# Kernel optimization log

Hardware: AMD Instinct MI355X
Metric: run time of the kernel (lower is better)

The kernel has to match this reference:

```python
import jax, jax.numpy as jnp
import numpy as np

V = 32000      # vocab_size
D = 768        # embed_dim / d_model
NL = 2         # attn_layers
BATCH = 2
T = 1024       # seq_len
ED = 2 * D     # d_inner (expand_factor=2)
NS = 16        # d_state
K = 4          # d_conv
DT_RANK = (D + 15) // 16  # ceil(d_model/16) = 48


def setup_inputs():
    key = jax.random.key(0)
    ks = jax.random.split(key, 12)
    nrm = lambda k, shp, s=0.02: (jax.random.normal(k, shp, jnp.float32) * s)
    tokens = jax.random.randint(ks[0], (BATCH, T), 0, V)
    embed = nrm(ks[1], (V, D))
    in_proj_w = nrm(ks[2], (NL, 2 * ED, D))
    conv_w = nrm(ks[3], (NL, ED, 1, K), 0.1)   # depthwise conv kernel (O=ED, I/g=1, K)
    conv_b = jnp.zeros((NL, ED), jnp.float32)
    x_proj_w = nrm(ks[4], (NL, DT_RANK + 2 * NS, ED))
    dt_proj_w = nrm(ks[5], (NL, ED, DT_RANK), 0.05)
    dt_proj_b = nrm(ks[6], (NL, ED), 0.05)
    # S4D real init: A = -[1..NS] per channel
    A_log = jnp.log(jnp.broadcast_to(jnp.arange(1, NS + 1, dtype=jnp.float32), (NL, ED, NS)))
    D_param = jnp.ones((NL, ED), jnp.float32)
    out_proj_w = nrm(ks[7], (NL, D, ED))
    ln_w = jnp.ones((NL, D), jnp.float32)
    ln_b = jnp.zeros((NL, D), jnp.float32)
    head_w = nrm(ks[8], (V, D))
    head_b = jnp.zeros((V,), jnp.float32)
    return {"tokens": tokens, "embed": embed, "in_proj_w": in_proj_w,
            "conv_w": conv_w, "conv_b": conv_b, "x_proj_w": x_proj_w,
            "dt_proj_w": dt_proj_w, "dt_proj_b": dt_proj_b, "A_log": A_log,
            "D_param": D_param, "out_proj_w": out_proj_w, "ln_w": ln_w,
            "ln_b": ln_b, "head_w": head_w, "head_b": head_b}


def silu(x):
    return x * jax.nn.sigmoid(x)


def layer_norm(x, w, b, eps=1e-5):
    mu = jnp.mean(x, axis=-1, keepdims=True)
    var = jnp.mean(jnp.square(x - mu), axis=-1, keepdims=True)
    return (x - mu) * jax.lax.rsqrt(var + eps) * w + b


def mamba_block(x, in_w, cw, cb, xp_w, dt_w, dt_b, a_log, d_par, out_w):
    # x: (B, T, D)
    xz = jnp.einsum('btd,ed->bte', x, in_w)           # (B, T, 2*ED)
    xin, z = jnp.split(xz, 2, axis=-1)                 # each (B, T, ED)
    # causal depthwise conv over time
    xc = jnp.transpose(xin, (0, 2, 1))                 # (B, ED, T)
    xc = jax.lax.conv_general_dilated(
        xc, cw, window_strides=(1,), padding=[(K - 1, 0)],
        dimension_numbers=('NCH', 'OIH', 'NCH'), feature_group_count=ED)
    xc = xc + cb[None, :, None]
    xin = silu(jnp.transpose(xc, (0, 2, 1)))           # (B, T, ED)
    # selective SSM
    A = -jnp.exp(a_log)                                # (ED, NS)
    dbc = jnp.einsum('bte,fe->btf', xin, xp_w)         # (B, T, dt_rank + 2*NS)
    delta = dbc[..., :DT_RANK]
    Bm = dbc[..., DT_RANK:DT_RANK + NS]                # (B, T, NS)
    Cm = dbc[..., DT_RANK + NS:]                       # (B, T, NS)
    delta = jax.nn.softplus(jnp.einsum('btr,er->bte', delta, dt_w) + dt_b)  # (B, T, ED)
    dA = jnp.exp(delta[..., None] * A)                 # (B, T, ED, NS)
    dBx = (delta * xin)[..., None] * Bm[:, :, None, :] # (B, T, ED, NS)

    def step(h, inp):
        dA_t, dBx_t, C_t = inp                         # (B,ED,NS),(B,ED,NS),(B,NS)
        h = dA_t * h + dBx_t
        y = jnp.einsum('ben,bn->be', h, C_t)
        return h, y

    h0 = jnp.zeros((x.shape[0], ED, NS), xin.dtype)
    _, ys = jax.lax.scan(step, h0,
                         (jnp.swapaxes(dA, 0, 1), jnp.swapaxes(dBx, 0, 1),
                          jnp.swapaxes(Cm, 0, 1)))
    y = jnp.swapaxes(ys, 0, 1) + d_par * xin           # (B, T, ED)
    return jnp.einsum('bte,de->btd', y * silu(z), out_w)


def reference(tokens, embed, in_proj_w, conv_w, conv_b, x_proj_w, dt_proj_w,
              dt_proj_b, A_log, D_param, out_proj_w, ln_w, ln_b, head_w, head_b):
    x = embed[tokens]                                  # (B, T, D)
    for l in range(NL):  # note: NO residual, matches x = ln(layer(x))
        x = layer_norm(
            mamba_block(x, in_proj_w[l], conv_w[l], conv_b[l], x_proj_w[l],
                        dt_proj_w[l], dt_proj_b[l], A_log[l], D_param[l],
                        out_proj_w[l]),
            ln_w[l], ln_b[l])
    return jnp.einsum('btd,vd->btv', x, head_w) + head_b
```

## Files before the change

### kernel.cpp

```cpp
#include <hip/hip_runtime.h>
#include <hip/hip_bf16.h>
#include <cstdint>
#include <cstddef>

using u16 = unsigned short;

#define DEV static __device__ __forceinline__

DEV float bf2f(u16 u) {
  unsigned int x = ((unsigned int)u) << 16;
  float f;
  __builtin_memcpy(&f, &x, 4);
  return f;
}

DEV u16 f2bf(float f) {
  unsigned int x;
  __builtin_memcpy(&x, &f, 4);
  unsigned int r = (x + 0x7fffu + ((x >> 16) & 1u)) >> 16;
  return (u16)r;
}

typedef __bf16 bf16x8 __attribute__((ext_vector_type(8)));
typedef float f32x4 __attribute__((ext_vector_type(4)));

DEV f32x4 mfma_bf16(bf16x8 a, bf16x8 b, f32x4 c) {
  return __builtin_amdgcn_mfma_f32_16x16x32_bf16(a, b, c, 0, 0, 0);
}

DEV void async_ld16(const void* g, void* lds) {
  __builtin_amdgcn_global_load_lds((const __attribute__((address_space(1))) void*)g,
                                   (__attribute__((address_space(3))) void*)lds,
                                   16, 0, 0);
}

__global__ __launch_bounds__(256) void k_cvt(const float* __restrict__ src,
                                             u16* __restrict__ dst, int n) {
  for (int i = blockIdx.x * 256 + threadIdx.x; i < n; i += gridDim.x * 256)
    dst[i] = f2bf(src[i]);
}

__global__ __launch_bounds__(256) void k_zero(float* __restrict__ p, int n) {
  const int i = blockIdx.x * 256 + threadIdx.x;
  if (i < n) p[i] = 0.f;
}

template <bool SPLIT, bool BIAS>
__global__ __launch_bounds__(512, 2) void gemm2(
    const u16* __restrict__ Ahi, const u16* __restrict__ Alo,
    const u16* __restrict__ Bw, float* __restrict__ Cf,
    const float* __restrict__ bias, int M, int N, int K, int ldc) {
  __shared__ __align__(16) u16 sA[2][128 * 64];
  __shared__ __align__(16) u16 sAl[SPLIT ? 2 : 1][128 * 64];
  __shared__ __align__(16) u16 sB[2][256 * 64];

  const int tid = threadIdx.x;
  const int wave = tid >> 6;
  const int lane = tid & 63;
  const int nwg = gridDim.x;
  const int w = (blockIdx.x & 7) * (nwg >> 3) + (blockIdx.x >> 3);
  const int mBlocks = M >> 7;
  const int mb = w % mBlocks;
  const int nb = w / mBlocks;
  const int mBase = mb * 128;
  const int nBase = nb * 256;
  const int wm = wave >> 2;
  const int wn = wave & 3;

  f32x4 acc[4][4];
#pragma unroll
  for (int i = 0; i < 4; ++i)
#pragma unroll
    for (int j = 0; j < 4; ++j) acc[i][j] = f32x4{0.f, 0.f, 0.f, 0.f};

  const int rl = lane >> 3;
  const int sw = (lane & 7) ^ rl;

  auto stage = [&](int bf, int k0) {
    const int koff = k0 + sw * 8;
#pragma unroll
    for (int r = 0; r < 2; ++r) {
      const int row = r * 64 + wave * 8;
      async_ld16(Ahi + (size_t)(mBase + row + rl) * K + koff,
                 (u16*)sA[bf] + row * 64);
    }
    if constexpr (SPLIT) {
#pragma unroll
      for (int r = 0; r < 2; ++r) {
        const int row = r * 64 + wave * 8;
        async_ld16(Alo + (size_t)(mBase + row + rl) * K + koff,
                   (u16*)sAl[bf] + row * 64);
      }
    }
#pragma unroll
    for (int r = 0; r < 4; ++r) {
      const int row = r * 64 + wave * 8;
      async_ld16(Bw + (size_t)(nBase + row + rl) * K + koff,
                 (u16*)sB[bf] + row * 64);
    }
  };

  const int rr = lane & 15;
  const int qh = lane >> 4;

  stage(0, 0);
  __syncthreads();

  const int nt = K >> 6;
  int cur = 0;
  for (int t = 0; t < nt; ++t) {
    if (t + 1 < nt) stage(cur ^ 1, (t + 1) * 64);
#pragma unroll
    for (int ph = 0; ph < 4; ++ph) {
      const int ks = (ph >> 1) * 32;
      const int ih = (ph & 1) * 2;
      const int q = (ks >> 3) + qh;
      bf16x8 aH[2], aL[2], bF[4];
#pragma unroll
      for (int i = 0; i < 2; ++i) {
        const int ra = wm * 64 + (ih + i) * 16 + rr;
        const int off = ra * 64 + ((q ^ (ra & 7)) << 3);
        aH[i] = *(const bf16x8*)((const u16*)sA[cur] + off);
        if constexpr (SPLIT) aL[i] = *(const bf16x8*)((const u16*)sAl[cur] + off);
      }
#pragma unroll
      for (int j = 0; j < 4; ++j) {
        const int rb = wn * 64 + j * 16 + rr;
        bF[j] = *(const bf16x8*)((const u16*)sB[cur] + rb * 64 + ((q ^ (rb & 7)) << 3));
      }
      __builtin_amdgcn_s_setprio(1);
#pragma unroll
      for (int i = 0; i < 2; ++i)
#pragma unroll
        for (int j = 0; j < 4; ++j) {
          acc[ih + i][j] = mfma_bf16(aH[i], bF[j], acc[ih + i][j]);
          if constexpr (SPLIT) acc[ih + i][j] = mfma_bf16(aL[i], bF[j], acc[ih + i][j]);
        }
      __builtin_amdgcn_s_setprio(0);
    }
    __syncthreads();
    cur ^= 1;
  }

  const int r0 = (lane >> 4) * 4;
  const int cn = lane & 15;
#pragma unroll
  for (int i = 0; i < 4; ++i) {
    const int mm = mBase + wm * 64 + i * 16 + r0;
#pragma unroll
    for (int j = 0; j < 4; ++j) {
      const int nn = nBase + wn * 64 + j * 16 + cn;
      float bv = 0.f;
      if constexpr (BIAS) bv = bias[nn];
#pragma unroll
      for (int r = 0; r < 4; ++r)
        Cf[(size_t)(mm + r) * ldc + nn] = acc[i][j][r] + bv;
    }
  }
}

template <bool SPLIT, bool BIAS, bool ATOMIC>
__global__ __launch_bounds__(256, 2) void gemm_bt(
    const u16* __restrict__ Ahi, const u16* __restrict__ Alo,
    const u16* __restrict__ Bw, float* __restrict__ Cf,
    const float* __restrict__ bias, int M, int N, int K, int ldc, int kChunk) {
  __shared__ __align__(16) u16 sA[128 * 64];
  __shared__ __align__(16) u16 sB[128 * 64];
  __shared__ __align__(16) u16 sAl[SPLIT ? 128 * 64 : 8];

  const int tid = threadIdx.x;
  const int wave = tid >> 6;
  const int lane = tid & 63;
  const int mBase = blockIdx.y * 128;
  const int nBase = blockIdx.x * 128;
  const int kBeg = blockIdx.z * kChunk;
  const int wm = wave >> 1;
  const int wn = wave & 1;

  f32x4 acc[4][4];
#pragma unroll
  for (int i = 0; i < 4; ++i)
#pragma unroll
    for (int j = 0; j < 4; ++j) acc[i][j] = f32x4{0.f, 0.f, 0.f, 0.f};

  const int rsub = lane >> 3;
  const int ksub = (lane & 7) * 8;

  for (int k0 = kBeg; k0 < kBeg + kChunk; k0 += 64) {
#pragma unroll
    for (int it = 0; it < 4; ++it) {
      const int chunk = it * 4 + wave;
      const int row = chunk * 8 + rsub;
      async_ld16(Ahi + (size_t)(mBase + row) * K + (k0 + ksub), (char*)sA + chunk * 1024);
      if constexpr (SPLIT)
        async_ld16(Alo + (size_t)(mBase + row) * K + (k0 + ksub), (char*)sAl + chunk * 1024);
      int rn = nBase + row;
      if (rn > N - 1) rn = N - 1;
      async_ld16(Bw + (size_t)rn * K + (k0 + ksub), (char*)sB + chunk * 1024);
    }
    __syncthreads();

    const int rr = lane & 15;
    const int q8 = (lane >> 4) * 8;
#pragma unroll
    for (int ks = 0; ks < 64; ks += 32) {
      bf16x8 aH[4], bF[4], aL[4];
#pragma unroll
      for (int i = 0; i < 4; ++i) {
        aH[i] = *(const bf16x8*)(sA + (wm * 64 + i * 16 + rr) * 64 + ks + q8);
        bF[i] = *(const bf16x8*)(sB + (wn * 64 + i * 16 + rr) * 64 + ks + q8);
        if constexpr (SPLIT)
          aL[i] = *(const bf16x8*)(sAl + (wm * 64 + i * 16 + rr) * 64 + ks + q8);
      }
#pragma unroll
      for (int i = 0; i < 4; ++i)
#pragma unroll
        for (int j = 0; j < 4; ++j) {
          acc[i][j] = mfma_bf16(aH[i], bF[j], acc[i][j]);
          if constexpr (SPLIT) acc[i][j] = mfma_bf16(aL[i], bF[j], acc[i][j]);
        }
    }
    __syncthreads();
  }

  const int r0 = (lane >> 4) * 4;
  const int cn = lane & 15;
#pragma unroll
  for (int i = 0; i < 4; ++i) {
    const int mm = mBase + wm * 64 + i * 16 + r0;
#pragma unroll
    for (int j = 0; j < 4; ++j) {
      const int nn = nBase + wn * 64 + j * 16 + cn;
      if (nn < N) {
        float bv = 0.f;
        if constexpr (BIAS) bv = bias[nn];
#pragma unroll
        for (int r = 0; r < 4; ++r) {
          if constexpr (ATOMIC)
            atomicAdd(&Cf[(size_t)(mm + r) * ldc + nn], acc[i][j][r]);
          else
            Cf[(size_t)(mm + r) * ldc + nn] = acc[i][j][r] + bv;
        }
      }
    }
  }
}

__global__ __launch_bounds__(256) void k_embed(const int* __restrict__ tok,
                                               const float* __restrict__ emb,
                                               u16* __restrict__ xh,
                                               u16* __restrict__ xl) {
  const int m = blockIdx.x;
  const float* src = emb + (size_t)tok[m] * 768;
  for (int d = threadIdx.x; d < 768; d += 256) {
    const float v = src[d];
    const u16 h = f2bf(v);
    xh[(size_t)m * 768 + d] = h;
    xl[(size_t)m * 768 + d] = f2bf(v - bf2f(h));
  }
}

__global__ __launch_bounds__(256) void k_conv(const float* __restrict__ xz,
                                              const float* __restrict__ cw,
                                              const float* __restrict__ cb,
                                              float* __restrict__ xinc,
                                              u16* __restrict__ xih,
                                              u16* __restrict__ xil) {
  const int idx = blockIdx.x * 256 + threadIdx.x;
  const int e = idx % 1536;
  const int m = idx / 1536;
  const int t = m & 1023;
  const int b = m >> 10;
  float acc = cb[e];
#pragma unroll
  for (int k = 0; k < 4; ++k) {
    const int tt = t - 3 + k;
    if (tt >= 0) acc += xz[(size_t)((b << 10) + tt) * 3072 + e] * cw[e * 4 + k];
  }
  const float s = acc / (1.f + __expf(-acc));
  xinc[idx] = s;
  const u16 h = f2bf(s);
  xih[idx] = h;
  xil[idx] = f2bf(s - bf2f(h));
}

__global__ __launch_bounds__(256) void k_dt(const float* __restrict__ dbc,
                                            const float* __restrict__ dtw,
                                            const float* __restrict__ dtb,
                                            float* __restrict__ delta) {
  const int m = blockIdx.x;
  __shared__ float sd[48];
  if (threadIdx.x < 48) sd[threadIdx.x] = dbc[m * 80 + threadIdx.x];
  __syncthreads();
  for (int e = threadIdx.x; e < 1536; e += 256) {
    float acc = dtb[e];
#pragma unroll
    for (int r = 0; r < 48; ++r) acc += sd[r] * dtw[e * 48 + r];
    const float sp = (acc > 20.f) ? acc : log1pf(__expf(acc));
    delta[m * 1536 + e] = sp;
  }
}

#define SCAN_NC 16
#define SCAN_CL 64

__global__ __launch_bounds__(256) void k_scan1(
    const float* __restrict__ delta, const float* __restrict__ xinc,
    const float* __restrict__ dbc, const float* __restrict__ alog,
    float* __restrict__ chP, float* __restrict__ chQ) {
  const int b = blockIdx.y;
  const int c = blockIdx.z;
  const int e = blockIdx.x * 16 + (threadIdx.x >> 4);
  const int n = threadIdx.x & 15;
  const float Aen = -__expf(alog[e * 16 + n]);
  const int m0 = (b << 10) + c * SCAN_CL;
  float h = 0.f, P = 1.f;
  float dl = delta[m0 * 1536 + e];
  float xi = xinc[m0 * 1536 + e];
  float Bn = dbc[m0 * 80 + 48 + n];
  for (int t = 0; t < SCAN_CL; ++t) {
    const float dl_c = dl, xi_c = xi, Bn_c = Bn;
    if (t < SCAN_CL - 1) {
      const int m2 = m0 + t + 1;
      dl = delta[m2 * 1536 + e];
      xi = xinc[m2 * 1536 + e];
      Bn = dbc[m2 * 80 + 48 + n];
    }
    const float dA = __expf(dl_c * Aen);
    P *= dA;
    h = dA * h + (dl_c * xi_c) * Bn_c;
  }
  const size_t idx = (((size_t)b * SCAN_NC + c) * 1536 + e) * 16 + n;
  chP[idx] = P;
  chQ[idx] = h;
}

__global__ __launch_bounds__(256) void k_scan_fix(const float* __restrict__ chP,
                                                  const float* __restrict__ chQ,
                                                  float* __restrict__ hst) {
  const int b = blockIdx.y;
  const int e = blockIdx.x * 16 + (threadIdx.x >> 4);
  const int n = threadIdx.x & 15;
  float h = 0.f;
#pragma unroll
  for (int c = 0; c < SCAN_NC; ++c) {
    const size_t idx = (((size_t)b * SCAN_NC + c) * 1536 + e) * 16 + n;
    hst[idx] = h;
    h = chP[idx] * h + chQ[idx];
  }
}

__global__ __launch_bounds__(256) void k_scan2(
    const float* __restrict__ delta, const float* __restrict__ xinc,
    const float* __restrict__ dbc, const float* __restrict__ xz,
    const float* __restrict__ alog, const float* __restrict__ dpar,
    const float* __restrict__ hst, u16* __restrict__ ymh,
    u16* __restrict__ yml) {
  const int b = blockIdx.y;
  const int c = blockIdx.z;
  const int e = blockIdx.x * 16 + (threadIdx.x >> 4);
  const int n = threadIdx.x & 15;
  const float Aen = -__expf(alog[e * 16 + n]);
  const float dp = dpar[e];
  const int m0 = (b << 10) + c * SCAN_CL;
  float h = hst[(((size_t)b * SCAN_NC + c) * 1536 + e) * 16 + n];
  float dl = delta[m0 * 1536 + e];
  float xi = xinc[m0 * 1536 + e];
  float Bn = dbc[m0 * 80 + 48 + n];
  float Cn = dbc[m0 * 80 + 64 + n];
  float zz = xz[(size_t)m0 * 3072 + 1536 + e];
  for (int t = 0; t < SCAN_CL; ++t) {
    const float dl_c = dl, xi_c = xi, Bn_c = Bn, Cn_c = Cn, zz_c = zz;
    if (t < SCAN_CL - 1) {
      const int m2 = m0 + t + 1;
      dl = delta[m2 * 1536 + e];
      xi = xinc[m2 * 1536 + e];
      Bn = dbc[m2 * 80 + 48 + n];
      Cn = dbc[m2 * 80 + 64 + n];
      zz = xz[(size_t)m2 * 3072 + 1536 + e];
    }
    const float dA = __expf(dl_c * Aen);
    h = dA * h + (dl_c * xi_c) * Bn_c;
    float p = h * Cn_c;
    p += __shfl_xor(p, 1);
    p += __shfl_xor(p, 2);
    p += __shfl_xor(p, 4);
    p += __shfl_xor(p, 8);
    if (n == 0) {
      const float y = p + dp * xi_c;
      const float sz = zz_c / (1.f + __expf(-zz_c));
      const float ym = y * sz;
      const int mt = m0 + t;
      const u16 hh = f2bf(ym);
      ymh[mt * 1536 + e] = hh;
      yml[mt * 1536 + e] = f2bf(ym - bf2f(hh));
    }
  }
}

__global__ __launch_bounds__(256) void k_ln(const float* __restrict__ g,
                                            const float* __restrict__ w,
                                            const float* __restrict__ bb,
                                            u16* __restrict__ xh,
                                            u16* __restrict__ xl) {
  const int m = blockIdx.x;
  const float* row = g + (size_t)m * 768;
  const int tid = threadIdx.x;
  const float v0 = row[tid], v1 = row[tid + 256], v2 = row[tid + 512];
  float s = v0 + v1 + v2;
#pragma unroll
  for (int o = 32; o > 0; o >>= 1) s += __shfl_xor(s, o);
  __shared__ float red[4];
  if ((tid & 63) == 0) red[tid >> 6] = s;
  __syncthreads();
  const float mu = (red[0] + red[1] + red[2] + red[3]) * (1.f / 768.f);
  const float d0 = v0 - mu, d1 = v1 - mu, d2 = v2 - mu;
  float q = d0 * d0 + d1 * d1 + d2 * d2;
#pragma unroll
  for (int o = 32; o > 0; o >>= 1) q += __shfl_xor(q, o);
  __syncthreads();
  if ((tid & 63) == 0) red[tid >> 6] = q;
  __syncthreads();
  const float var = (red[0] + red[1] + red[2] + red[3]) * (1.f / 768.f);
  const float rs = rsqrtf(var + 1e-5f);
  const float dd[3] = {d0, d1, d2};
#pragma unroll
  for (int i = 0; i < 3; ++i) {
    const int d = tid + i * 256;
    const float y = dd[i] * rs * w[d] + bb[d];
    const u16 h = f2bf(y);
    xh[(size_t)m * 768 + d] = h;
    xl[(size_t)m * 768 + d] = f2bf(y - bf2f(h));
  }
}

extern "C" void kernel_launch(void* const* d_in, const int* in_sizes, int n_in,
                              void* d_out, int out_size, void* d_ws, size_t ws_size,
                              hipStream_t stream) {
  const int* tokens = (const int*)d_in[0];
  const float* embed = (const float*)d_in[1];
  const float* in_w = (const float*)d_in[2];
  const float* conv_w = (const float*)d_in[3];
  const float* conv_b = (const float*)d_in[4];
  const float* xp_w = (const float*)d_in[5];
  const float* dt_w = (const float*)d_in[6];
  const float* dt_b = (const float*)d_in[7];
  const float* A_log = (const float*)d_in[8];
  const float* D_par = (const float*)d_in[9];
  const float* out_w = (const float*)d_in[10];
  const float* ln_w = (const float*)d_in[11];
  const float* ln_b = (const float*)d_in[12];
  const float* head_w = (const float*)d_in[13];
  const float* head_b = (const float*)d_in[14];

  char* p = (char*)d_ws;
  auto alloc = [&](size_t bytes) {
    char* r = p;
    p += (bytes + 255) & ~(size_t)255;
    return r;
  };
  float* xz = (float*)alloc(2048ull * 3072 * 4);
  float* xinc = (float*)alloc(2048ull * 1536 * 4);
  u16* xih = (u16*)alloc(2048ull * 1536 * 2);
  u16* xil = (u16*)alloc(2048ull * 1536 * 2);
  float* dbc = (float*)alloc(2048ull * 80 * 4);
  float* delta = (float*)alloc(2048ull * 1536 * 4);
  u16* ymh = (u16*)alloc(2048ull * 1536 * 2);
  u16* yml = (u16*)alloc(2048ull * 1536 * 2);
  float* gout = (float*)alloc(2048ull * 768 * 4);
  u16* xh = (u16*)alloc(2048ull * 768 * 2);
  u16* xl = (u16*)alloc(2048ull * 768 * 2);
  u16* w_in_h = (u16*)alloc(2ull * 3072 * 768 * 2);
  u16* w_xp_h = (u16*)alloc(2ull * 80 * 1536 * 2);
  u16* w_out_h = (u16*)alloc(2ull * 768 * 1536 * 2);
  u16* w_head_h = (u16*)alloc(32000ull * 768 * 2);
  float* chP = (float*)alloc(2ull * SCAN_NC * 1536 * 16 * 4);
  float* chQ = (float*)alloc(2ull * SCAN_NC * 1536 * 16 * 4);
  float* hst = (float*)alloc(2ull * SCAN_NC * 1536 * 16 * 4);

  k_cvt<<<2048, 256, 0, stream>>>(in_w, w_in_h, 2 * 3072 * 768);
  k_cvt<<<256, 256, 0, stream>>>(xp_w, w_xp_h, 2 * 80 * 1536);
  k_cvt<<<1024, 256, 0, stream>>>(out_w, w_out_h, 2 * 768 * 1536);
  k_cvt<<<4096, 256, 0, stream>>>(head_w, w_head_h, 32000 * 768);

  k_embed<<<2048, 256, 0, stream>>>(tokens, embed, xh, xl);

  for (int l = 0; l < 2; ++l) {
    gemm2<true, false><<<12 * 16, 512, 0, stream>>>(
        xh, xl, w_in_h + (size_t)l * 2359296, xz, nullptr, 2048, 3072, 768, 3072);

    k_conv<<<12288, 256, 0, stream>>>(xz, conv_w + l * 6144, conv_b + l * 1536, xinc, xih, xil);

    k_zero<<<640, 256, 0, stream>>>(dbc, 2048 * 80);
    gemm_bt<true, false, true><<<dim3(1, 16, 12), 256, 0, stream>>>(
        xih, xil, w_xp_h + (size_t)l * 122880, dbc, nullptr, 2048, 80, 1536, 80, 128);

    k_dt<<<2048, 256, 0, stream>>>(dbc, dt_w + (size_t)l * 73728, dt_b + l * 1536, delta);

    k_scan1<<<dim3(96, 2, SCAN_NC), 256, 0, stream>>>(
        delta, xinc, dbc, A_log + l * 24576, chP, chQ);
    k_scan_fix<<<dim3(96, 2), 256, 0, stream>>>(chP, chQ, hst);
    k_scan2<<<dim3(96, 2, SCAN_NC), 256, 0, stream>>>(
        delta, xinc, dbc, xz, A_log + l * 24576, D_par + l * 1536, hst, ymh, yml);

    k_zero<<<6144, 256, 0, stream>>>(gout, 2048 * 768);
    gemm_bt<true, false, true><<<dim3(6, 16, 8), 256, 0, stream>>>(
        ymh, yml, w_out_h + (size_t)l * 1179648, gout, nullptr, 2048, 768, 1536, 768, 192);

    k_ln<<<2048, 256, 0, stream>>>(gout, ln_w + l * 768, ln_b + l * 768, xh, xl);
  }

  gemm2<true, true><<<125 * 16, 512, 0, stream>>>(
      xh, xl, w_head_h, (float*)d_out, head_b, 2048, 32000, 768, 32000);
}
```

Baseline: 1.289 ms.

## Interleave hi/lo bf16 activations along K and triple-buffer GEMM pipeline

Activations split into bf16 hi and lo parts are now stored side by side in one row of width 2K, and the GEMMs loop over the doubled K while wrapping the weight index. This replaces paired MFMAs on separate hi/lo tiles with a single MFMA stream. The main GEMM moves from double to triple buffering, using explicit vmcnt waits and raw barriers so two stages of loads are in flight. The four weight-conversion launches are merged into one kernel, and gemm_bt's occupancy hint is raised to 4 blocks per CU. The extra LDS from the third buffer and the hand-written waitcnt counts add risk to occupancy and to correctness of the synchronisation.

```diff
diff --git a/kernel.cpp b/kernel.cpp
--- a/kernel.cpp
+++ b/kernel.cpp
@@ -34,10 +34,28 @@
                                    16, 0, 0);
 }
 
-__global__ __launch_bounds__(256) void k_cvt(const float* __restrict__ src,
-                                             u16* __restrict__ dst, int n) {
-  for (int i = blockIdx.x * 256 + threadIdx.x; i < n; i += gridDim.x * 256)
-    dst[i] = f2bf(src[i]);
+DEV void hard_barrier() {
+  __builtin_amdgcn_sched_barrier(0);
+  __builtin_amdgcn_s_barrier();
+  __builtin_amdgcn_sched_barrier(0);
+}
+
+__global__ __launch_bounds__(256) void k_cvt_all(
+    const float* __restrict__ s0, u16* __restrict__ d0, int n0,
+    const float* __restrict__ s1, u16* __restrict__ d1, int n1,
+    const float* __restrict__ s2, u16* __restrict__ d2, int n2,
+    const float* __restrict__ s3, u16* __restrict__ d3, int n3) {
+  const int total = n0 + n1 + n2 + n3;
+  for (int i = blockIdx.x * 256 + threadIdx.x; i < total; i += gridDim.x * 256) {
+    int j = i;
+    if (j < n0) { d0[j] = f2bf(s0[j]); continue; }
+    j -= n0;
+    if (j < n1) { d1[j] = f2bf(s1[j]); continue; }
+    j -= n1;
+    if (j < n2) { d2[j] = f2bf(s2[j]); continue; }
+    j -= n2;
+    d3[j] = f2bf(s3[j]);
+  }
 }
 
 __global__ __launch_bounds__(256) void k_zero(float* __restrict__ p, int n) {
@@ -45,14 +63,13 @@
   if (i < n) p[i] = 0.f;
 }
 
-template <bool SPLIT, bool BIAS>
-__global__ __launch_bounds__(512, 2) void gemm2(
-    const u16* __restrict__ Ahi, const u16* __restrict__ Alo,
-    const u16* __restrict__ Bw, float* __restrict__ Cf,
-    const float* __restrict__ bias, int M, int N, int K, int ldc) {
-  __shared__ __align__(16) u16 sA[2][128 * 64];
-  __shared__ __align__(16) u16 sAl[SPLIT ? 2 : 1][128 * 64];
-  __shared__ __align__(16) u16 sB[2][256 * 64];
+template <bool BIAS>
+__global__ __launch_bounds__(512, 2) void gemm3(
+    const u16* __restrict__ A, const u16* __restrict__ Bw,
+    float* __restrict__ Cf, const float* __restrict__ bias,
+    int M, int N, int K, int K0, int ldc) {
+  __shared__ __align__(16) u16 sA[3 * 128 * 64];
+  __shared__ __align__(16) u16 sB[3 * 256 * 64];
 
   const int tid = threadIdx.x;
   const int wave = tid >> 6;
@@ -76,70 +93,70 @@
   const int rl = lane >> 3;
   const int sw = (lane & 7) ^ rl;
 
-  auto stage = [&](int bf, int k0) {
-    const int koff = k0 + sw * 8;
+  auto stage = [&](int bf, int kt) {
+    const int k0 = kt * 64;
+    const int ka = k0 + sw * 8;
+    const int kb = (k0 >= K0 ? k0 - K0 : k0) + sw * 8;
+    u16* dA = sA + bf * (128 * 64);
+    u16* dB = sB + bf * (256 * 64);
 #pragma unroll
     for (int r = 0; r < 2; ++r) {
       const int row = r * 64 + wave * 8;
-      async_ld16(Ahi + (size_t)(mBase + row + rl) * K + koff,
-                 (u16*)sA[bf] + row * 64);
-    }
-    if constexpr (SPLIT) {
-#pragma unroll
-      for (int r = 0; r < 2; ++r) {
-        const int row = r * 64 + wave * 8;
-        async_ld16(Alo + (size_t)(mBase + row + rl) * K + koff,
-                   (u16*)sAl[bf] + row * 64);
-      }
+      async_ld16(A + (size_t)(mBase + row + rl) * K + ka, dA + row * 64);
     }
 #pragma unroll
     for (int r = 0; r < 4; ++r) {
       const int row = r * 64 + wave * 8;
-      async_ld16(Bw + (size_t)(nBase + row + rl) * K + koff,
-                 (u16*)sB[bf] + row * 64);
+      async_ld16(Bw + (size_t)(nBase + row + rl) * K0 + kb, dB + row * 64);
     }
   };
+
+  const int nt = K >> 6;
+  stage(0, 0);
+  stage(1, 1);
+  asm volatile("s_waitcnt vmcnt(6)" ::: "memory");
+  hard_barrier();
 
   const int rr = lane & 15;
   const int qh = lane >> 4;
 
-  stage(0, 0);
-  __syncthreads();
-
-  const int nt = K >> 6;
-  int cur = 0;
+  int p = 0, ps = 2;
   for (int t = 0; t < nt; ++t) {
-    if (t + 1 < nt) stage(cur ^ 1, (t + 1) * 64);
-#pragma unroll
-    for (int ph = 0; ph < 4; ++ph) {
-      const int ks = (ph >> 1) * 32;
-      const int ih = (ph & 1) * 2;
-      const int q = (ks >> 3) + qh;
-      bf16x8 aH[2], aL[2], bF[4];
-#pragma unroll
-      for (int i = 0; i < 2; ++i) {
-        const int ra = wm * 64 + (ih + i) * 16 + rr;
-        const int off = ra * 64 + ((q ^ (ra & 7)) << 3);
-        aH[i] = *(const bf16x8*)((const u16*)sA[cur] + off);
-        if constexpr (SPLIT) aL[i] = *(const bf16x8*)((const u16*)sAl[cur] + off);
+    if (t + 2 < nt) stage(ps, t + 2);
+    const u16* bA = sA + p * (128 * 64);
+    const u16* bB = sB + p * (256 * 64);
+#pragma unroll
+    for (int ks = 0; ks < 2; ++ks) {
+      const int q = ks * 4 + qh;
+      bf16x8 aF[4], bF[4];
+#pragma unroll
+      for (int i = 0; i < 4; ++i) {
+        const int ra = wm * 64 + i * 16 + rr;
+        aF[i] = *(const bf16x8*)(bA + ra * 64 + ((q ^ (ra & 7)) << 3));
       }
 #pragma unroll
       for (int j = 0; j < 4; ++j) {
         const int rb = wn * 64 + j * 16 + rr;
-        bF[j] = *(const bf16x8*)((const u16*)sB[cur] + rb * 64 + ((q ^ (rb & 7)) << 3));
+        bF[j] = *(const bf16x8*)(bB + rb * 64 + ((q ^ (rb & 7)) << 3));
       }
       __builtin_amdgcn_s_setprio(1);
 #pragma unroll
-      for (int i = 0; i < 2; ++i)
-#pragma unroll
-        for (int j = 0; j < 4; ++j) {
-          acc[ih + i][j] = mfma_bf16(aH[i], bF[j], acc[ih + i][j]);
-          if constexpr (SPLIT) acc[ih + i][j] = mfma_bf16(aL[i], bF[j], acc[ih + i][j]);
-        }
+      for (int i = 0; i < 4; ++i)
+#pragma unroll
+        for (int j = 0; j < 4; ++j)
+          acc[i][j] = mfma_bf16(aF[i], bF[j], acc[i][j]);
       __builtin_amdgcn_s_setprio(0);
     }
-    __syncthreads();
-    cur ^= 1;
+    if (t + 1 < nt) {
+      if (t + 3 <= nt) {
+        asm volatile("s_waitcnt vmcnt(6)" ::: "memory");
+      } else {
+        asm volatile("s_waitcnt vmcnt(0)" ::: "memory");
+      }
+      hard_barrier();
+    }
+    p = (p == 2) ? 0 : p + 1;
+    ps = (ps == 2) ? 0 : ps + 1;
   }
 
   const int r0 = (lane >> 4) * 4;
@@ -159,14 +176,13 @@
   }
 }
 
-template <bool SPLIT, bool BIAS, bool ATOMIC>
-__global__ __launch_bounds__(256, 2) void gemm_bt(
-    const u16* __restrict__ Ahi, const u16* __restrict__ Alo,
-    const u16* __restrict__ Bw, float* __restrict__ Cf,
-    const float* __restrict__ bias, int M, int N, int K, int ldc, int kChunk) {
+template <bool BIAS, bool ATOMIC>
+__global__ __launch_bounds__(256, 4) void gemm_bt(
+    const u16* __restrict__ Ahi, const u16* __restrict__ Bw,
+    float* __restrict__ Cf, const float* __restrict__ bias,
+    int M, int N, int K, int K0, int ldc, int kChunk) {
   __shared__ __align__(16) u16 sA[128 * 64];
   __shared__ __align__(16) u16 sB[128 * 64];
-  __shared__ __align__(16) u16 sAl[SPLIT ? 128 * 64 : 8];
 
   const int tid = threadIdx.x;
   const int wave = tid >> 6;
@@ -187,16 +203,15 @@
   const int ksub = (lane & 7) * 8;
 
   for (int k0 = kBeg; k0 < kBeg + kChunk; k0 += 64) {
+    const int kb = (k0 >= K0) ? k0 - K0 : k0;
 #pragma unroll
     for (int it = 0; it < 4; ++it) {
       const int chunk = it * 4 + wave;
       const int row = chunk * 8 + rsub;
       async_ld16(Ahi + (size_t)(mBase + row) * K + (k0 + ksub), (char*)sA + chunk * 1024);
-      if constexpr (SPLIT)
-        async_ld16(Alo + (size_t)(mBase + row) * K + (k0 + ksub), (char*)sAl + chunk * 1024);
       int rn = nBase + row;
       if (rn > N - 1) rn = N - 1;
-      async_ld16(Bw + (size_t)rn * K + (k0 + ksub), (char*)sB + chunk * 1024);
+      async_ld16(Bw + (size_t)rn * K0 + (kb + ksub), (char*)sB + chunk * 1024);
     }
     __syncthreads();
 
@@ -204,21 +219,17 @@
     const int q8 = (lane >> 4) * 8;
 #pragma unroll
     for (int ks = 0; ks < 64; ks += 32) {
-      bf16x8 aH[4], bF[4], aL[4];
+      bf16x8 aH[4], bF[4];
 #pragma unroll
       for (int i = 0; i < 4; ++i) {
         aH[i] = *(const bf16x8*)(sA + (wm * 64 + i * 16 + rr) * 64 + ks + q8);
         bF[i] = *(const bf16x8*)(sB + (wn * 64 + i * 16 + rr) * 64 + ks + q8);
-        if constexpr (SPLIT)
-          aL[i] = *(const bf16x8*)(sAl + (wm * 64 + i * 16 + rr) * 64 + ks + q8);
       }
 #pragma unroll
       for (int i = 0; i < 4; ++i)
 #pragma unroll
-        for (int j = 0; j < 4; ++j) {
+        for (int j = 0; j < 4; ++j)
           acc[i][j] = mfma_bf16(aH[i], bF[j], acc[i][j]);
-          if constexpr (SPLIT) acc[i][j] = mfma_bf16(aL[i], bF[j], acc[i][j]);
-        }
     }
     __syncthreads();
   }
@@ -248,15 +259,14 @@
 
 __global__ __launch_bounds__(256) void k_embed(const int* __restrict__ tok,
                                                const float* __restrict__ emb,
-                                               u16* __restrict__ xh,
-                                               u16* __restrict__ xl) {
+                                               u16* __restrict__ xhl) {
   const int m = blockIdx.x;
   const float* src = emb + (size_t)tok[m] * 768;
   for (int d = threadIdx.x; d < 768; d += 256) {
     const float v = src[d];
     const u16 h = f2bf(v);
-    xh[(size_t)m * 768 + d] = h;
-    xl[(size_t)m * 768 + d] = f2bf(v - bf2f(h));
+    xhl[(size_t)m * 1536 + d] = h;
+    xhl[(size_t)m * 1536 + 768 + d] = f2bf(v - bf2f(h));
   }
 }
 
@@ -264,8 +274,7 @@
                                               const float* __restrict__ cw,
                                               const float* __restrict__ cb,
                                               float* __restrict__ xinc,
-                                              u16* __restrict__ xih,
-                                              u16* __restrict__ xil) {
+                                              u16* __restrict__ xihl) {
   const int idx = blockIdx.x * 256 + threadIdx.x;
   const int e = idx % 1536;
   const int m = idx / 1536;
@@ -280,8 +289,8 @@
   const float s = acc / (1.f + __expf(-acc));
   xinc[idx] = s;
   const u16 h = f2bf(s);
-  xih[idx] = h;
-  xil[idx] = f2bf(s - bf2f(h));
+  xihl[(size_t)m * 3072 + e] = h;
+  xihl[(size_t)m * 3072 + 1536 + e] = f2bf(s - bf2f(h));
 }
 
 __global__ __launch_bounds__(256) void k_dt(const float* __restrict__ dbc,
@@ -354,8 +363,7 @@
     const float* __restrict__ delta, const float* __restrict__ xinc,
     const float* __restrict__ dbc, const float* __restrict__ xz,
     const float* __restrict__ alog, const float* __restrict__ dpar,
-    const float* __restrict__ hst, u16* __restrict__ ymh,
-    u16* __restrict__ yml) {
+    const float* __restrict__ hst, u16* __restrict__ ymhl) {
   const int b = blockIdx.y;
   const int c = blockIdx.z;
   const int e = blockIdx.x * 16 + (threadIdx.x >> 4);
@@ -392,8 +400,8 @@
       const float ym = y * sz;
       const int mt = m0 + t;
       const u16 hh = f2bf(ym);
-      ymh[mt * 1536 + e] = hh;
-      yml[mt * 1536 + e] = f2bf(ym - bf2f(hh));
+      ymhl[(size_t)mt * 3072 + e] = hh;
+      ymhl[(size_t)mt * 3072 + 1536 + e] = f2bf(ym - bf2f(hh));
     }
   }
 }
@@ -401,8 +409,7 @@
 __global__ __launch_bounds__(256) void k_ln(const float* __restrict__ g,
                                             const float* __restrict__ w,
                                             const float* __restrict__ bb,
-                                            u16* __restrict__ xh,
-                                            u16* __restrict__ xl) {
+                                            u16* __restrict__ xhl) {
   const int m = blockIdx.x;
   const float* row = g + (size_t)m * 768;
   const int tid = threadIdx.x;
@@ -429,8 +436,8 @@
     const int d = tid + i * 256;
     const float y = dd[i] * rs * w[d] + bb[d];
     const u16 h = f2bf(y);
-    xh[(size_t)m * 768 + d] = h;
-    xl[(size_t)m * 768 + d] = f2bf(y - bf2f(h));
+    xhl[(size_t)m * 1536 + d] = h;
+    xhl[(size_t)m * 1536 + 768 + d] = f2bf(y - bf2f(h));
   }
 }
 
@@ -461,15 +468,12 @@
   };
   float* xz = (float*)alloc(2048ull * 3072 * 4);
   float* xinc = (float*)alloc(2048ull * 1536 * 4);
-  u16* xih = (u16*)alloc(2048ull * 1536 * 2);
-  u16* xil = (u16*)alloc(2048ull * 1536 * 2);
+  u16* xihl = (u16*)alloc(2048ull * 3072 * 2);
   float* dbc = (float*)alloc(2048ull * 80 * 4);
   float* delta = (float*)alloc(2048ull * 1536 * 4);
-  u16* ymh = (u16*)alloc(2048ull * 1536 * 2);
-  u16* yml = (u16*)alloc(2048ull * 1536 * 2);
+  u16* ymhl = (u16*)alloc(2048ull * 3072 * 2);
   float* gout = (float*)alloc(2048ull * 768 * 4);
-  u16* xh = (u16*)alloc(2048ull * 768 * 2);
-  u16* xl = (u16*)alloc(2048ull * 768 * 2);
+  u16* xhl = (u16*)alloc(2048ull * 1536 * 2);
   u16* w_in_h = (u16*)alloc(2ull * 3072 * 768 * 2);
   u16* w_xp_h = (u16*)alloc(2ull * 80 * 1536 * 2);
   u16* w_out_h = (u16*)alloc(2ull * 768 * 1536 * 2);
@@ -478,22 +482,22 @@
   float* chQ = (float*)alloc(2ull * SCAN_NC * 1536 * 16 * 4);
   float* hst = (float*)alloc(2ull * SCAN_NC * 1536 * 16 * 4);
 
-  k_cvt<<<2048, 256, 0, stream>>>(in_w, w_in_h, 2 * 3072 * 768);
-  k_cvt<<<256, 256, 0, stream>>>(xp_w, w_xp_h, 2 * 80 * 1536);
-  k_cvt<<<1024, 256, 0, stream>>>(out_w, w_out_h, 2 * 768 * 1536);
-  k_cvt<<<4096, 256, 0, stream>>>(head_w, w_head_h, 32000 * 768);
-
-  k_embed<<<2048, 256, 0, stream>>>(tokens, embed, xh, xl);
+  k_cvt_all<<<4096, 256, 0, stream>>>(in_w, w_in_h, 2 * 3072 * 768,
+                                      xp_w, w_xp_h, 2 * 80 * 1536,
+                                      out_w, w_out_h, 2 * 768 * 1536,
+                                      head_w, w_head_h, 32000 * 768);
+
+  k_embed<<<2048, 256, 0, stream>>>(tokens, embed, xhl);
 
   for (int l = 0; l < 2; ++l) {
-    gemm2<true, false><<<12 * 16, 512, 0, stream>>>(
-        xh, xl, w_in_h + (size_t)l * 2359296, xz, nullptr, 2048, 3072, 768, 3072);
-
-    k_conv<<<12288, 256, 0, stream>>>(xz, conv_w + l * 6144, conv_b + l * 1536, xinc, xih, xil);
+    gemm3<false><<<192, 512, 0, stream>>>(
+        xhl, w_in_h + (size_t)l * 2359296, xz, nullptr, 2048, 3072, 1536, 768, 3072);
+
+    k_conv<<<12288, 256, 0, stream>>>(xz, conv_w + l * 6144, conv_b + l * 1536, xinc, xihl);
 
     k_zero<<<640, 256, 0, stream>>>(dbc, 2048 * 80);
-    gemm_bt<true, false, true><<<dim3(1, 16, 12), 256, 0, stream>>>(
-        xih, xil, w_xp_h + (size_t)l * 122880, dbc, nullptr, 2048, 80, 1536, 80, 128);
+    gemm_bt<false, true><<<dim3(1, 16, 12), 256, 0, stream>>>(
+        xihl, w_xp_h + (size_t)l * 122880, dbc, nullptr, 2048, 80, 3072, 1536, 80, 256);
 
     k_dt<<<2048, 256, 0, stream>>>(dbc, dt_w + (size_t)l * 73728, dt_b + l * 1536, delta);
 
@@ -501,15 +505,15 @@
         delta, xinc, dbc, A_log + l * 24576, chP, chQ);
     k_scan_fix<<<dim3(96, 2), 256, 0, stream>>>(chP, chQ, hst);
     k_scan2<<<dim3(96, 2, SCAN_NC), 256, 0, stream>>>(
-        delta, xinc, dbc, xz, A_log + l * 24576, D_par + l * 1536, hst, ymh, yml);
+        delta, xinc, dbc, xz, A_log + l * 24576, D_par + l * 1536, hst, ymhl);
 
     k_zero<<<6144, 256, 0, stream>>>(gout, 2048 * 768);
-    gemm_bt<true, false, true><<<dim3(6, 16, 8), 256, 0, stream>>>(
-        ymh, yml, w_out_h + (size_t)l * 1179648, gout, nullptr, 2048, 768, 1536, 768, 192);
-
-    k_ln<<<2048, 256, 0, stream>>>(gout, ln_w + l * 768, ln_b + l * 768, xh, xl);
-  }
-
-  gemm2<true, true><<<125 * 16, 512, 0, stream>>>(
-      xh, xl, w_head_h, (float*)d_out, head_b, 2048, 32000, 768, 32000);
-}
+    gemm_bt<false, true><<<dim3(6, 16, 8), 256, 0, stream>>>(
+        ymhl, w_out_h + (size_t)l * 1179648, gout, nullptr, 2048, 768, 3072, 1536, 768, 384);
+
+    k_ln<<<2048, 256, 0, stream>>>(gout, ln_w + l * 768, ln_b + l * 768, xhl);
+  }
+
+  gemm3<true><<<2000, 512, 0, stream>>>(
+      xhl, w_head_h, (float*)d_out, head_b, 2048, 32000, 1536, 768, 32000);
+}
```

Measured after the change: 1.348 ms. 1.05x slower.
